# Performance work log

Hardware: AMD Instinct MI355X
Metric: run time of the kernel (lower is better)

Reference implementation:

```python
import jax, jax.numpy as jnp
import numpy as np

B, T, C = 2, 2048, 2048
H, HD = 16, 128          # n_head, head_dim
LORA = C // 4            # kv_lora_rank = n_embd // compression_ratio
RD = HD // 2             # qk_rope_dim
ND = HD - RD             # qk_nope_dim
THETA = 100000.0


def setup_inputs() -> dict:
    key = jax.random.key(0)
    k0, k1, k2, k3, k4 = jax.random.split(key, 5)
    s = 0.02
    return {
        "x": jax.random.normal(k0, (B, T, C), dtype=jnp.float32),
        "Wq": jax.random.normal(k1, (C, H * HD), dtype=jnp.float32) * s,
        "Wkva": jax.random.normal(k2, (C, LORA + RD), dtype=jnp.float32) * s,
        "Wkvb": jax.random.normal(k3, (LORA, H * ND), dtype=jnp.float32) * s,
        "Wo": jax.random.normal(k4, (H * HD, C), dtype=jnp.float32) * s,
    }


def apply_rope(x, theta=THETA):
    # x: [B, H, T, D] with D even; interleaved complex rotation (torch.view_as_complex style)
    b, h, t, d = x.shape
    freqs = 1.0 / (theta ** (jnp.arange(0, d, 2, dtype=jnp.float32) / d))  # [D/2]
    ang = jnp.arange(t, dtype=jnp.float32)[:, None] * freqs[None, :]       # [T, D/2]
    cos, sin = jnp.cos(ang), jnp.sin(ang)
    xr = x.reshape(b, h, t, d // 2, 2)
    x0, x1 = xr[..., 0], xr[..., 1]
    o0 = x0 * cos - x1 * sin
    o1 = x0 * sin + x1 * cos
    return jnp.stack([o0, o1], axis=-1).reshape(b, h, t, d)


def reference(x, Wq, Wkva, Wkvb, Wo):
    Bx, Tx, Cx = x.shape
    # query projection -> [B, H, T, HD]
    q = (x @ Wq).reshape(Bx, Tx, H, HD).transpose(0, 2, 1, 3)
    # compressed KV + shared (MQA) rope key
    ckv = x @ Wkva                                  # [B, T, LORA+RD]
    kv_latent = ckv[..., :LORA]                     # [B, T, LORA]
    k_rope = ckv[..., LORA:]                        # [B, T, RD]
    # decompress nope part of K (== nope part of V)
    kv = (kv_latent @ Wkvb).reshape(Bx, Tx, H, ND).transpose(0, 2, 1, 3)  # [B,H,T,ND]
    k_rope = jnp.broadcast_to(k_rope[:, None, :, :], (Bx, H, Tx, RD))
    q_nope, q_rope = q[..., :ND], q[..., ND:]
    q_rope = apply_rope(q_rope)
    k_rope = apply_rope(k_rope)
    qf = jnp.concatenate([q_nope, q_rope], axis=-1)               # [B,H,T,HD]
    kf = jnp.concatenate([kv, k_rope], axis=-1)                   # [B,H,T,HD]
    vf = jnp.concatenate([kv, jnp.zeros_like(k_rope)], axis=-1)   # [B,H,T,HD]
    scale = 1.0 / np.sqrt(HD).astype(np.float32)
    att = jnp.einsum("bhtd,bhsd->bhts", qf, kf) * scale           # [B,H,T,T]
    causal = jnp.tril(jnp.ones((Tx, Tx), dtype=bool))
    att = jnp.where(causal, att, -jnp.inf)
    att = jax.nn.softmax(att, axis=-1)
    y = jnp.einsum("bhts,bhsd->bhtd", att, vf)                    # [B,H,T,HD]
    y = y.transpose(0, 2, 1, 3).reshape(Bx, Tx, H * HD)
    return y @ Wo
```

## Files before the change

kernel.cpp:

```cpp
#include <hip/hip_runtime.h>
#include <hip/hip_bf16.h>
#include <math.h>

#define B_ 2
#define T_ 2048
#define C_ 2048
#define H_ 16
#define HD_ 128
#define LORA_ 512
#define RD_ 64
#define ND_ 64
#define BT_ (B_*T_)
#define NKVA_ 576
#define NKVAP_ 640
#define LOG2_THETA 16.609640474436812f

typedef __bf16 bf16x8 __attribute__((ext_vector_type(8)));
typedef float  f32x4  __attribute__((ext_vector_type(4)));

#define MFMA16(a,b,c) __builtin_amdgcn_mfma_f32_16x16x32_bf16((a),(b),(c),0,0,0)

__device__ static inline void load_lds16(const __bf16* g, __bf16* l) {
  auto* lp = (__attribute__((address_space(3))) char*)(uintptr_t)(l);
  auto* gp = (const __attribute__((address_space(1))) char*)(g);
  __builtin_amdgcn_global_load_lds(gp, lp, 16, 0, 0);
}

__device__ static inline unsigned pkbf(float a, float b) {
  union { __bf16 h[2]; unsigned u; } v;
  v.h[0] = (__bf16)a; v.h[1] = (__bf16)b;
  return v.u;
}

__global__ __launch_bounds__(256) void k_cast_x(const float* __restrict__ x,
                                                __bf16* __restrict__ xb, int n) {
  int idx = blockIdx.x * 256 + threadIdx.x;
  if (idx < n) xb[idx] = (__bf16)x[idx];
}

__global__ __launch_bounds__(256) void k_tcast(const float* __restrict__ src,
                                               __bf16* __restrict__ dst,
                                               int K, int N, int NP) {
  __shared__ float tile[32][33];
  int k0 = blockIdx.x * 32;
  int n0 = blockIdx.y * 32;
  int tx = threadIdx.x & 31, ty = threadIdx.x >> 5;
  for (int i = ty; i < 32; i += 8) {
    int n = n0 + tx;
    tile[i][tx] = (n < N) ? src[(size_t)(k0 + i) * N + n] : 0.0f;
  }
  __syncthreads();
  for (int i = ty; i < 32; i += 8) {
    dst[(size_t)(n0 + i) * K + k0 + tx] = (__bf16)tile[tx][i];
  }
}

__global__ __launch_bounds__(256) void k_tcast_wo(const float* __restrict__ Wo,
                                                  __bf16* __restrict__ dst) {
  __shared__ float tile[32][33];
  int kc0 = blockIdx.x * 32;
  int n0  = blockIdx.y * 32;
  int rbase = (kc0 >> 6) * 128 + (kc0 & 63);
  int tx = threadIdx.x & 31, ty = threadIdx.x >> 5;
  for (int i = ty; i < 32; i += 8)
    tile[i][tx] = Wo[(size_t)(rbase + i) * C_ + n0 + tx];
  __syncthreads();
  for (int i = ty; i < 32; i += 8)
    dst[(size_t)(n0 + i) * 1024 + kc0 + tx] = (__bf16)tile[tx][i];
}

__global__ __launch_bounds__(256) void k_gemm_bt(const __bf16* __restrict__ A,
                                                 const __bf16* __restrict__ B,
                                                 float* __restrict__ C,
                                                 int M, int N, int K) {
  __shared__ __align__(16) __bf16 As[2][128 * 32];
  __shared__ __align__(16) __bf16 Bs[2][128 * 32];
  const int tid  = threadIdx.x;
  const int lane = tid & 63;
  const int wave = tid >> 6;
  const int bm = blockIdx.x, bn = blockIdx.y;
  const int r0 = tid >> 2;
  const int c8 = (tid & 3) * 8;
  const __bf16* Ag = A + (size_t)(bm * 128 + r0) * K + c8;
  const __bf16* Bg = B + (size_t)(bn * 128 + r0) * K + c8;
  const int wr = (wave >> 1) * 64, wc = (wave & 1) * 64;
  const int fr = lane & 15, fk = (lane >> 4) * 8;
  const f32x4 fzero = {0.f, 0.f, 0.f, 0.f};
  f32x4 acc[4][4];
#pragma unroll
  for (int i = 0; i < 4; ++i)
#pragma unroll
    for (int j = 0; j < 4; ++j) acc[i][j] = fzero;

  load_lds16(Ag,                  &As[0][tid * 8]);
  load_lds16(Ag + (size_t)64 * K, &As[0][tid * 8 + 2048]);
  load_lds16(Bg,                  &Bs[0][tid * 8]);
  load_lds16(Bg + (size_t)64 * K, &Bs[0][tid * 8 + 2048]);

  int buf = 0;
  for (int k0 = 0; k0 < K; k0 += 32) {
    __syncthreads();
    if (k0 + 32 < K) {
      const int nb = buf ^ 1;
      load_lds16(Ag + k0 + 32,                  &As[nb][tid * 8]);
      load_lds16(Ag + (size_t)64 * K + k0 + 32, &As[nb][tid * 8 + 2048]);
      load_lds16(Bg + k0 + 32,                  &Bs[nb][tid * 8]);
      load_lds16(Bg + (size_t)64 * K + k0 + 32, &Bs[nb][tid * 8 + 2048]);
    }
    bf16x8 af[4], bfg[4];
#pragma unroll
    for (int i = 0; i < 4; ++i) af[i]  = *(const bf16x8*)&As[buf][(wr + i * 16 + fr) * 32 + fk];
#pragma unroll
    for (int j = 0; j < 4; ++j) bfg[j] = *(const bf16x8*)&Bs[buf][(wc + j * 16 + fr) * 32 + fk];
#pragma unroll
    for (int i = 0; i < 4; ++i)
#pragma unroll
      for (int j = 0; j < 4; ++j)
        acc[i][j] = MFMA16(af[i], bfg[j], acc[i][j]);
    buf ^= 1;
  }
  const int rbase = (lane >> 4) * 4;
  float* Cb = C + (size_t)(bm * 128 + wr + rbase) * N + bn * 128 + wc + fr;
#pragma unroll
  for (int i = 0; i < 4; ++i)
#pragma unroll
    for (int j = 0; j < 4; ++j)
#pragma unroll
      for (int r = 0; r < 4; ++r)
        Cb[(size_t)(i * 16 + r) * N + j * 16] = acc[i][j][r];
}

__global__ __launch_bounds__(256) void k_rope_q(const float* __restrict__ q,
                                                __bf16* __restrict__ qf) {
  const float scale2 = 1.4426950408889634f / 11.313708498984760f;
  int idx = blockIdx.x * 256 + threadIdx.x;
  int d  = idx & 127;
  int t  = (idx >> 7) & 2047;
  int bh = idx >> 18;
  int h  = bh & 15, b = bh >> 4;
  const float* qrow = q + ((size_t)(b * T_ + t)) * 2048 + h * 128;
  float v;
  if (d < 64) {
    v = qrow[d];
  } else {
    int i = (d - 64) >> 1;
    float freq = exp2f(-((float)(2 * i) / 64.0f) * LOG2_THETA);
    float ang = (float)t * freq;
    float c = cosf(ang), s = sinf(ang);
    float x0 = qrow[64 + 2 * i], x1 = qrow[64 + 2 * i + 1];
    v = (d & 1) ? (x0 * s + x1 * c) : (x0 * c - x1 * s);
  }
  qf[idx] = (__bf16)(v * scale2);
}

__global__ __launch_bounds__(256) void k_rope_kf(const float* __restrict__ ckv,
                                                 __bf16* __restrict__ kf) {
  int idx = blockIdx.x * 256 + threadIdx.x;
  int d = idx & 63;
  int t = (idx >> 6) & 2047;
  int h = (idx >> 17) & 15;
  int b = idx >> 21;
  const float* src = ckv + ((size_t)(b * T_ + t)) * NKVAP_ + 512;
  int i = d >> 1;
  float freq = exp2f(-((float)(2 * i) / 64.0f) * LOG2_THETA);
  float ang = (float)t * freq;
  float c = cosf(ang), s = sinf(ang);
  float x0 = src[2 * i], x1 = src[2 * i + 1];
  float v = (d & 1) ? (x0 * s + x1 * c) : (x0 * c - x1 * s);
  kf[(((size_t)(b * H_ + h)) * T_ + t) * 128 + 64 + d] = (__bf16)v;
}

__global__ __launch_bounds__(256) void k_cast_kvl(const float* __restrict__ ckv,
                                                  __bf16* __restrict__ kvl) {
  int idx = blockIdx.x * 256 + threadIdx.x;
  int r = idx >> 9, c = idx & 511;
  kvl[idx] = (__bf16)ckv[(size_t)r * NKVAP_ + c];
}

__global__ __launch_bounds__(256) void k_pack_kv(const float* __restrict__ kv,
                                                 __bf16* __restrict__ kf,
                                                 __bf16* __restrict__ kvT) {
  __shared__ float tile[64][65];
  const int bh = blockIdx.x;
  const int b = bh >> 4, h = bh & 15;
  const int t0 = blockIdx.y * 64;
  const int tid = threadIdx.x;
  const int i0 = tid >> 4, d4 = (tid & 15) * 4;
#pragma unroll
  for (int p = 0; p < 4; ++p) {
    int i = i0 + p * 16;
    const float* src = kv + ((size_t)(b * T_ + t0 + i)) * 1024 + h * 64 + d4;
    float4 v = *(const float4*)src;
    tile[i][d4] = v.x; tile[i][d4 + 1] = v.y; tile[i][d4 + 2] = v.z; tile[i][d4 + 3] = v.w;
    union { __bf16 hh[4]; uint2 u; } o;
    o.hh[0] = (__bf16)v.x; o.hh[1] = (__bf16)v.y; o.hh[2] = (__bf16)v.z; o.hh[3] = (__bf16)v.w;
    *(uint2*)(kf + ((size_t)bh * T_ + t0 + i) * 128 + d4) = o.u;
  }
  __syncthreads();
  const int dd = tid >> 2, tc0 = (tid & 3) * 16;
  __bf16 outv[16];
#pragma unroll
  for (int j = 0; j < 16; ++j) outv[j] = (__bf16)tile[tc0 + j][dd];
  __bf16* dst = kvT + ((size_t)(bh * 64 + dd)) * T_ + t0 + tc0;
  *(bf16x8*)dst = *(bf16x8*)&outv[0];
  *(bf16x8*)(dst + 8) = *(bf16x8*)&outv[8];
}

__global__ __launch_bounds__(256, 4) void k_attn(const __bf16* __restrict__ qf,
                                                 const __bf16* __restrict__ kf,
                                                 const __bf16* __restrict__ kvT,
                                                 __bf16* __restrict__ yc) {
  const int blk = blockIdx.x;
  const int bh = blk & 31;
  const int qt = 31 - (blk >> 5);
  const int b = bh >> 4, h = bh & 15;
  const int qbase = qt * 64;
  const int tid = threadIdx.x;
  const int lane = tid & 63, wave = tid >> 6;
  const int fr = lane & 15, quad = lane >> 4, fk8 = quad * 8;

  __shared__ __align__(16) __bf16 Ks[64][136];
  __shared__ __align__(16) __bf16 VsT[64][72];

  const int qi = qbase + wave * 16 + fr;
  const __bf16* qb = qf + ((size_t)bh * T_ + qi) * HD_;
  bf16x8 aq[4];
#pragma unroll
  for (int g = 0; g < 4; ++g) aq[g] = *(const bf16x8*)(qb + g * 32 + fk8);

  const f32x4 fzero = {0.f, 0.f, 0.f, 0.f};
  f32x4 accO[4];
#pragma unroll
  for (int g = 0; g < 4; ++g) accO[g] = fzero;
  float m = -1e30f, l = 0.f;

  const int srow = tid >> 4, scol = (tid & 15) * 8;
  const int vrow = tid >> 3, vcol = (tid & 7) * 8;
  const __bf16* kbh = kf + (size_t)bh * T_ * 128;
  const __bf16* vbh = kvT + (size_t)bh * 64 * T_;
  const int srcA = (quad & 1) * 32 + fr, srcB = srcA + 16;
  const int hi = quad >> 1;

  bf16x8 kreg[4], vreg[2];
#pragma unroll
  for (int p = 0; p < 4; ++p)
    kreg[p] = *(const bf16x8*)(kbh + (size_t)(srow + p * 16) * 128 + scol);
#pragma unroll
  for (int p = 0; p < 2; ++p)
    vreg[p] = *(const bf16x8*)(vbh + (size_t)(vrow + p * 32) * T_ + vcol);

  for (int s0 = 0; s0 <= qbase; s0 += 64) {
    __syncthreads();
#pragma unroll
    for (int p = 0; p < 4; ++p) *(bf16x8*)&Ks[srow + p * 16][scol] = kreg[p];
#pragma unroll
    for (int p = 0; p < 2; ++p) *(bf16x8*)&VsT[vrow + p * 32][vcol] = vreg[p];
    __syncthreads();

    if (s0 < qbase) {
      const int sn = s0 + 64;
#pragma unroll
      for (int p = 0; p < 4; ++p)
        kreg[p] = *(const bf16x8*)(kbh + (size_t)(sn + srow + p * 16) * 128 + scol);
#pragma unroll
      for (int p = 0; p < 2; ++p)
        vreg[p] = *(const bf16x8*)(vbh + (size_t)(vrow + p * 32) * T_ + sn + vcol);
    }

    f32x4 accST[4];
#pragma unroll
    for (int cg = 0; cg < 4; ++cg) accST[cg] = fzero;
    __builtin_amdgcn_s_setprio(1);
#pragma unroll
    for (int cg = 0; cg < 4; ++cg) {
#pragma unroll
      for (int kg = 0; kg < 4; ++kg) {
        bf16x8 bk = *(const bf16x8*)&Ks[cg * 16 + fr][kg * 32 + fk8];
        accST[cg] = MFMA16(bk, aq[kg], accST[cg]);
      }
    }
    __builtin_amdgcn_s_setprio(0);

    float lmax = -1e30f;
    if (s0 == qbase) {
#pragma unroll
      for (int cg = 0; cg < 4; ++cg) {
#pragma unroll
        for (int r = 0; r < 4; ++r) {
          const int key = s0 + cg * 16 + quad * 4 + r;
          float v = accST[cg][r];
          v = (key <= qi) ? v : -1e30f;
          accST[cg][r] = v;
          lmax = fmaxf(lmax, v);
        }
      }
    } else {
#pragma unroll
      for (int cg = 0; cg < 4; ++cg) {
#pragma unroll
        for (int r = 0; r < 4; ++r) lmax = fmaxf(lmax, accST[cg][r]);
      }
    }
    lmax = fmaxf(lmax, __shfl_xor(lmax, 16, 64));
    lmax = fmaxf(lmax, __shfl_xor(lmax, 32, 64));
    const float mn = fmaxf(m, lmax);
    const float alpha = exp2f(m - mn);
    m = mn;

    float lsum = 0.f;
    unsigned pk0[4], pk1[4];
#pragma unroll
    for (int cg = 0; cg < 4; ++cg) {
      float p0 = exp2f(accST[cg][0] - m);
      float p1 = exp2f(accST[cg][1] - m);
      float p2 = exp2f(accST[cg][2] - m);
      float p3 = exp2f(accST[cg][3] - m);
      lsum += (p0 + p1) + (p2 + p3);
      pk0[cg] = pkbf(p0, p1);
      pk1[cg] = pkbf(p2, p3);
    }
    lsum += __shfl_xor(lsum, 16, 64);
    lsum += __shfl_xor(lsum, 32, 64);
    l = l * alpha + lsum;
#pragma unroll
    for (int g = 0; g < 4; ++g)
#pragma unroll
      for (int r = 0; r < 4; ++r) accO[g][r] *= alpha;

#pragma unroll
    for (int ks = 0; ks < 2; ++ks) {
      int a0 = __shfl((int)pk0[2 * ks], srcA, 64);
      int b0 = __shfl((int)pk0[2 * ks + 1], srcA, 64);
      int a1 = __shfl((int)pk1[2 * ks], srcA, 64);
      int b1 = __shfl((int)pk1[2 * ks + 1], srcA, 64);
      int a2 = __shfl((int)pk0[2 * ks], srcB, 64);
      int b2 = __shfl((int)pk0[2 * ks + 1], srcB, 64);
      int a3 = __shfl((int)pk1[2 * ks], srcB, 64);
      int b3 = __shfl((int)pk1[2 * ks + 1], srcB, 64);
      union { int i[4]; bf16x8 v; } pf;
      pf.i[0] = hi ? b0 : a0;
      pf.i[1] = hi ? b1 : a1;
      pf.i[2] = hi ? b2 : a2;
      pf.i[3] = hi ? b3 : a3;
      __builtin_amdgcn_s_setprio(1);
#pragma unroll
      for (int g = 0; g < 4; ++g) {
        bf16x8 vv = *(const bf16x8*)&VsT[g * 16 + fr][ks * 32 + fk8];
        accO[g] = MFMA16(vv, pf.v, accO[g]);
      }
      __builtin_amdgcn_s_setprio(0);
    }
  }

  const float linv = 1.0f / l;
  __bf16* yb = yc + ((size_t)(b * T_ + qi)) * 1024 + h * 64 + quad * 4;
#pragma unroll
  for (int g = 0; g < 4; ++g) {
    union { unsigned u[2]; uint2 v; } o;
    o.u[0] = pkbf(accO[g][0] * linv, accO[g][1] * linv);
    o.u[1] = pkbf(accO[g][2] * linv, accO[g][3] * linv);
    *(uint2*)(yb + g * 16) = o.v;
  }
}

extern "C" void kernel_launch(void* const* d_in, const int* in_sizes, int n_in,
                              void* d_out, int out_size, void* d_ws, size_t ws_size,
                              hipStream_t stream) {
  const float* x    = (const float*)d_in[0];
  const float* Wq   = (const float*)d_in[1];
  const float* Wkva = (const float*)d_in[2];
  const float* Wkvb = (const float*)d_in[3];
  const float* Wo   = (const float*)d_in[4];
  float* out = (float*)d_out;
  char* ws = (char*)d_ws;

  size_t off = 0;
  __bf16* xb    = (__bf16*)(ws + off); off += (size_t)BT_ * C_ * 2;
  __bf16* WqT   = (__bf16*)(ws + off); off += (size_t)2048 * 2048 * 2;
  __bf16* WkvaT = (__bf16*)(ws + off); off += (size_t)NKVAP_ * 2048 * 2;
  __bf16* WkvbT = (__bf16*)(ws + off); off += (size_t)1024 * 512 * 2;
  __bf16* WoTc  = (__bf16*)(ws + off); off += (size_t)2048 * 1024 * 2;
  float*  q     = (float*)(ws + off);  off += (size_t)BT_ * 2048 * 4;
  float*  ckv   = (float*)(ws + off);  off += (size_t)BT_ * NKVAP_ * 4;
  __bf16* kvl   = (__bf16*)(ws + off); off += (size_t)BT_ * 512 * 2;
  float*  kv    = (float*)(ws + off);  off += (size_t)BT_ * 1024 * 4;
  __bf16* qfb   = (__bf16*)(ws + off); off += (size_t)B_ * H_ * T_ * HD_ * 2;
  __bf16* yc    = (__bf16*)(ws + off); off += (size_t)BT_ * 1024 * 2;
  __bf16* kfb = (__bf16*)q;
  __bf16* kvT = (__bf16*)((char*)q + (size_t)B_ * H_ * T_ * HD_ * 2);

  k_cast_x<<<(BT_ * C_) / 256, 256, 0, stream>>>(x, xb, BT_ * C_);
  k_tcast<<<dim3(2048 / 32, 2048 / 32), 256, 0, stream>>>(Wq, WqT, 2048, 2048, 2048);
  k_tcast<<<dim3(2048 / 32, NKVAP_ / 32), 256, 0, stream>>>(Wkva, WkvaT, 2048, NKVA_, NKVAP_);
  k_tcast<<<dim3(512 / 32, 1024 / 32), 256, 0, stream>>>(Wkvb, WkvbT, 512, 1024, 1024);
  k_tcast_wo<<<dim3(1024 / 32, 2048 / 32), 256, 0, stream>>>(Wo, WoTc);

  k_gemm_bt<<<dim3(BT_ / 128, 2048 / 128), 256, 0, stream>>>(xb, WqT, q, BT_, 2048, 2048);
  k_gemm_bt<<<dim3(BT_ / 128, NKVAP_ / 128), 256, 0, stream>>>(xb, WkvaT, ckv, BT_, NKVAP_, 2048);

  k_rope_q<<<(B_ * H_ * T_ * HD_) / 256, 256, 0, stream>>>(q, qfb);
  k_cast_kvl<<<(BT_ * 512) / 256, 256, 0, stream>>>(ckv, kvl);

  k_gemm_bt<<<dim3(BT_ / 128, 1024 / 128), 256, 0, stream>>>(kvl, WkvbT, kv, BT_, 1024, 512);
  k_pack_kv<<<dim3(B_ * H_, T_ / 64), 256, 0, stream>>>(kv, kfb, kvT);
  k_rope_kf<<<(B_ * H_ * T_ * 64) / 256, 256, 0, stream>>>(ckv, kfb);

  k_attn<<<(T_ / 64) * B_ * H_, 256, 0, stream>>>(qfb, kfb, kvT, yc);

  k_gemm_bt<<<dim3(BT_ / 128, 2048 / 128), 256, 0, stream>>>(yc, WoTc, out, BT_, 2048, 1024);
}
```

Measured before the change: 348.8 us.

## Load attention K/V tiles directly from global into registers, dropping LDS staging

The attention kernel no longer stages K and V tiles through shared memory with a register prefetch and two barriers per tile. Each wave now loads its own MFMA operand fragments straight from global memory (K before the score MFMAs, V before the softmax) and feeds them to the MFMAs. This removes the LDS writes and reads and the __syncthreads, but all four waves now fetch the same K/V data redundantly through the cache. The loads are also no longer prefetched a tile ahead, so their latency is exposed unless occupancy hides it.

Measured after the change: 494.5 us. +41.8%, slower.

```diff
diff --git a/kernel.cpp b/kernel.cpp
--- a/kernel.cpp
+++ b/kernel.cpp
@@ -219,9 +219,6 @@
   const int lane = tid & 63, wave = tid >> 6;
   const int fr = lane & 15, quad = lane >> 4, fk8 = quad * 8;
 
-  __shared__ __align__(16) __bf16 Ks[64][136];
-  __shared__ __align__(16) __bf16 VsT[64][72];
-
   const int qi = qbase + wave * 16 + fr;
   const __bf16* qb = qf + ((size_t)bh * T_ + qi) * HD_;
   bf16x8 aq[4];
@@ -234,38 +231,18 @@
   for (int g = 0; g < 4; ++g) accO[g] = fzero;
   float m = -1e30f, l = 0.f;
 
-  const int srow = tid >> 4, scol = (tid & 15) * 8;
-  const int vrow = tid >> 3, vcol = (tid & 7) * 8;
   const __bf16* kbh = kf + (size_t)bh * T_ * 128;
   const __bf16* vbh = kvT + (size_t)bh * 64 * T_;
   const int srcA = (quad & 1) * 32 + fr, srcB = srcA + 16;
   const int hi = quad >> 1;
 
-  bf16x8 kreg[4], vreg[2];
-#pragma unroll
-  for (int p = 0; p < 4; ++p)
-    kreg[p] = *(const bf16x8*)(kbh + (size_t)(srow + p * 16) * 128 + scol);
-#pragma unroll
-  for (int p = 0; p < 2; ++p)
-    vreg[p] = *(const bf16x8*)(vbh + (size_t)(vrow + p * 32) * T_ + vcol);
-
   for (int s0 = 0; s0 <= qbase; s0 += 64) {
-    __syncthreads();
-#pragma unroll
-    for (int p = 0; p < 4; ++p) *(bf16x8*)&Ks[srow + p * 16][scol] = kreg[p];
-#pragma unroll
-    for (int p = 0; p < 2; ++p) *(bf16x8*)&VsT[vrow + p * 32][vcol] = vreg[p];
-    __syncthreads();
-
-    if (s0 < qbase) {
-      const int sn = s0 + 64;
-#pragma unroll
-      for (int p = 0; p < 4; ++p)
-        kreg[p] = *(const bf16x8*)(kbh + (size_t)(sn + srow + p * 16) * 128 + scol);
-#pragma unroll
-      for (int p = 0; p < 2; ++p)
-        vreg[p] = *(const bf16x8*)(vbh + (size_t)(vrow + p * 32) * T_ + sn + vcol);
-    }
+    bf16x8 kr[4][4];
+#pragma unroll
+    for (int cg = 0; cg < 4; ++cg)
+#pragma unroll
+      for (int kg = 0; kg < 4; ++kg)
+        kr[cg][kg] = *(const bf16x8*)(kbh + (size_t)(s0 + cg * 16 + fr) * 128 + kg * 32 + fk8);
 
     f32x4 accST[4];
 #pragma unroll
@@ -274,12 +251,17 @@
 #pragma unroll
     for (int cg = 0; cg < 4; ++cg) {
 #pragma unroll
-      for (int kg = 0; kg < 4; ++kg) {
-        bf16x8 bk = *(const bf16x8*)&Ks[cg * 16 + fr][kg * 32 + fk8];
-        accST[cg] = MFMA16(bk, aq[kg], accST[cg]);
-      }
+      for (int kg = 0; kg < 4; ++kg)
+        accST[cg] = MFMA16(kr[cg][kg], aq[kg], accST[cg]);
     }
     __builtin_amdgcn_s_setprio(0);
+
+    bf16x8 vr[4][2];
+#pragma unroll
+    for (int g = 0; g < 4; ++g)
+#pragma unroll
+      for (int ks = 0; ks < 2; ++ks)
+        vr[g][ks] = *(const bf16x8*)(vbh + (size_t)(g * 16 + fr) * T_ + s0 + ks * 32 + fk8);
 
     float lmax = -1e30f;
     if (s0 == qbase) {
@@ -344,10 +326,8 @@
       pf.i[3] = hi ? b3 : a3;
       __builtin_amdgcn_s_setprio(1);
 #pragma unroll
-      for (int g = 0; g < 4; ++g) {
-        bf16x8 vv = *(const bf16x8*)&VsT[g * 16 + fr][ks * 32 + fk8];
-        accO[g] = MFMA16(vv, pf.v, accO[g]);
-      }
+      for (int g = 0; g < 4; ++g)
+        accO[g] = MFMA16(vr[g][ks], pf.v, accO[g]);
       __builtin_amdgcn_s_setprio(0);
     }
   }
```

## Double-buffer K/V LDS tiles with XOR swizzle and lazy softmax rescaling

Applied to the files above, without the earlier changes.

Switches the attention kernel's K and V shared-memory tiles to double buffering, so each iteration needs one barrier instead of two and the next tile is written while the current one is consumed. Padding is dropped in favour of an XOR swizzle to avoid LDS bank conflicts. The online-softmax rescale of the accumulator is skipped unless some row's max exceeds the running max by more than a threshold, saving exp and multiply work. It doubles LDS use and lowers the occupancy hint from 4 to 3 blocks per SIMD, and the lazy rescale relies on bounded growth of the exponentials in fp32.

After: 343.5 us. No clear change (-1.5%).

```diff
diff --git a/kernel.cpp b/kernel.cpp
--- a/kernel.cpp
+++ b/kernel.cpp
@@ -206,7 +206,7 @@
   *(bf16x8*)(dst + 8) = *(bf16x8*)&outv[8];
 }
 
-__global__ __launch_bounds__(256, 4) void k_attn(const __bf16* __restrict__ qf,
+__global__ __launch_bounds__(256, 3) void k_attn(const __bf16* __restrict__ qf,
                                                  const __bf16* __restrict__ kf,
                                                  const __bf16* __restrict__ kvT,
                                                  __bf16* __restrict__ yc) {
@@ -219,8 +219,8 @@
   const int lane = tid & 63, wave = tid >> 6;
   const int fr = lane & 15, quad = lane >> 4, fk8 = quad * 8;
 
-  __shared__ __align__(16) __bf16 Ks[64][136];
-  __shared__ __align__(16) __bf16 VsT[64][72];
+  __shared__ __align__(16) __bf16 Ks[2][64 * 128];
+  __shared__ __align__(16) __bf16 Vs[2][64 * 64];
 
   const int qi = qbase + wave * 16 + fr;
   const __bf16* qb = qf + ((size_t)bh * T_ + qi) * HD_;
@@ -234,38 +234,43 @@
   for (int g = 0; g < 4; ++g) accO[g] = fzero;
   float m = -1e30f, l = 0.f;
 
-  const int srow = tid >> 4, scol = (tid & 15) * 8;
-  const int vrow = tid >> 3, vcol = (tid & 7) * 8;
+  const int srow = tid >> 4, scolh = (tid & 15) * 8;
+  const int vrow = tid >> 3, vcolh = (tid & 7) * 8;
+  const int kwcol = scolh ^ ((srow & 7) * 8);
+  const int vwcol = vcolh ^ ((vrow & 7) * 8);
+  const int kswz = (fr & 7) * 8;
   const __bf16* kbh = kf + (size_t)bh * T_ * 128;
   const __bf16* vbh = kvT + (size_t)bh * 64 * T_;
   const int srcA = (quad & 1) * 32 + fr, srcB = srcA + 16;
   const int hi = quad >> 1;
 
   bf16x8 kreg[4], vreg[2];
-#pragma unroll
-  for (int p = 0; p < 4; ++p)
-    kreg[p] = *(const bf16x8*)(kbh + (size_t)(srow + p * 16) * 128 + scol);
-#pragma unroll
-  for (int p = 0; p < 2; ++p)
-    vreg[p] = *(const bf16x8*)(vbh + (size_t)(vrow + p * 32) * T_ + vcol);
-
+  auto load_regs = [&](int S) {
+#pragma unroll
+    for (int p = 0; p < 4; ++p)
+      kreg[p] = *(const bf16x8*)(kbh + (size_t)(S + srow + p * 16) * 128 + scolh);
+#pragma unroll
+    for (int p = 0; p < 2; ++p)
+      vreg[p] = *(const bf16x8*)(vbh + (size_t)(vrow + p * 32) * T_ + S + vcolh);
+  };
+  auto write_buf = [&](int bufi) {
+#pragma unroll
+    for (int p = 0; p < 4; ++p)
+      *(bf16x8*)&Ks[bufi][(srow + p * 16) * 128 + kwcol] = kreg[p];
+#pragma unroll
+    for (int p = 0; p < 2; ++p)
+      *(bf16x8*)&Vs[bufi][(vrow + p * 32) * 64 + vwcol] = vreg[p];
+  };
+
+  load_regs(0);
+  write_buf(0);
+  if (qbase > 0) load_regs(64);
+  __syncthreads();
+
+  int cur = 0;
   for (int s0 = 0; s0 <= qbase; s0 += 64) {
-    __syncthreads();
-#pragma unroll
-    for (int p = 0; p < 4; ++p) *(bf16x8*)&Ks[srow + p * 16][scol] = kreg[p];
-#pragma unroll
-    for (int p = 0; p < 2; ++p) *(bf16x8*)&VsT[vrow + p * 32][vcol] = vreg[p];
-    __syncthreads();
-
-    if (s0 < qbase) {
-      const int sn = s0 + 64;
-#pragma unroll
-      for (int p = 0; p < 4; ++p)
-        kreg[p] = *(const bf16x8*)(kbh + (size_t)(sn + srow + p * 16) * 128 + scol);
-#pragma unroll
-      for (int p = 0; p < 2; ++p)
-        vreg[p] = *(const bf16x8*)(vbh + (size_t)(vrow + p * 32) * T_ + sn + vcol);
-    }
+    if (s0 + 64 <= qbase) write_buf(cur ^ 1);
+    if (s0 + 128 <= qbase) load_regs(s0 + 128);
 
     f32x4 accST[4];
 #pragma unroll
@@ -275,7 +280,7 @@
     for (int cg = 0; cg < 4; ++cg) {
 #pragma unroll
       for (int kg = 0; kg < 4; ++kg) {
-        bf16x8 bk = *(const bf16x8*)&Ks[cg * 16 + fr][kg * 32 + fk8];
+        bf16x8 bk = *(const bf16x8*)&Ks[cur][(cg * 16 + fr) * 128 + ((kg * 32 + fk8) ^ kswz)];
         accST[cg] = MFMA16(bk, aq[kg], accST[cg]);
       }
     }
@@ -303,9 +308,17 @@
     }
     lmax = fmaxf(lmax, __shfl_xor(lmax, 16, 64));
     lmax = fmaxf(lmax, __shfl_xor(lmax, 32, 64));
-    const float mn = fmaxf(m, lmax);
-    const float alpha = exp2f(m - mn);
-    m = mn;
+
+    if (!__all(lmax <= m + 8.0f)) {
+      const float mn = fmaxf(m, lmax);
+      const float alpha = exp2f(m - mn);
+      l *= alpha;
+#pragma unroll
+      for (int g = 0; g < 4; ++g)
+#pragma unroll
+        for (int r = 0; r < 4; ++r) accO[g][r] *= alpha;
+      m = mn;
+    }
 
     float lsum = 0.f;
     unsigned pk0[4], pk1[4];
@@ -321,11 +334,7 @@
     }
     lsum += __shfl_xor(lsum, 16, 64);
     lsum += __shfl_xor(lsum, 32, 64);
-    l = l * alpha + lsum;
-#pragma unroll
-    for (int g = 0; g < 4; ++g)
-#pragma unroll
-      for (int r = 0; r < 4; ++r) accO[g][r] *= alpha;
+    l += lsum;
 
 #pragma unroll
     for (int ks = 0; ks < 2; ++ks) {
@@ -345,11 +354,14 @@
       __builtin_amdgcn_s_setprio(1);
 #pragma unroll
       for (int g = 0; g < 4; ++g) {
-        bf16x8 vv = *(const bf16x8*)&VsT[g * 16 + fr][ks * 32 + fk8];
+        bf16x8 vv = *(const bf16x8*)&Vs[cur][(g * 16 + fr) * 64 + ((ks * 32 + fk8) ^ kswz)];
         accO[g] = MFMA16(vv, pf.v, accO[g]);
       }
       __builtin_amdgcn_s_setprio(0);
     }
+
+    __syncthreads();
+    cur ^= 1;
   }
 
   const float linv = 1.0f / l;
```
